# Kernel tuning notes

Measured on AMD Instinct MI355X. Metric: run time of the kernel, lower is better.

## Reference

```python
import jax, jax.numpy as jnp
import numpy as np

B, C_IN, T_IN = 128, 128, 2500
C_OUT, K, STRIDE, PAD = 64, 27, 4, 13  # T_out = 625
BN_EPS = 1e-5
SURROGATE_ALPHA = 4.0


def binarize_weight(w):
    """1-bit (XNOR-Net style) weight quantization with straight-through estimator.
    w: (O, I, K). Per-output-channel scale = mean |w|."""
    alpha = jnp.mean(jnp.abs(w), axis=(1, 2), keepdims=True)
    wq = jnp.sign(w) * alpha
    return w + jax.lax.stop_gradient(wq - w)


def spike(x):
    """Heaviside spike with sigmoid surrogate gradient (STE)."""
    hard = (x > 0).astype(x.dtype)
    soft = jax.nn.sigmoid(SURROGATE_ALPHA * x)
    return soft + jax.lax.stop_gradient(hard - soft)


def setup_inputs() -> dict:
    key = jax.random.key(0)
    ks = jax.random.split(key, 8)
    scale_conv = 1.0 / np.sqrt(C_IN * K)
    scale_lin = 1.0 / np.sqrt(C_OUT)
    return {
        "x": jax.random.normal(ks[0], (B, C_IN, T_IN), dtype=jnp.float32),
        "conv_w": jax.random.normal(ks[1], (C_OUT, C_IN, K), dtype=jnp.float32) * scale_conv,
        "conv_b": jnp.zeros((C_OUT,), dtype=jnp.float32),
        "bn_gamma": jnp.ones((C_OUT,), dtype=jnp.float32),
        "bn_beta": jnp.zeros((C_OUT,), dtype=jnp.float32),
        "bn_mean": jax.random.normal(ks[2], (C_OUT,), dtype=jnp.float32) * 0.1,
        "bn_var": jax.random.uniform(ks[3], (C_OUT,), dtype=jnp.float32, minval=0.5, maxval=1.5),
        "wq": jax.random.normal(ks[4], (C_OUT, C_OUT), dtype=jnp.float32) * scale_lin,
        "wk": jax.random.normal(ks[5], (C_OUT, C_OUT), dtype=jnp.float32) * scale_lin,
        "wv": jax.random.normal(ks[6], (C_OUT, C_OUT), dtype=jnp.float32) * scale_lin,
        "wo": jax.random.normal(ks[7], (C_OUT, C_OUT), dtype=jnp.float32) * scale_lin,
    }


def reference(x, conv_w, conv_b, bn_gamma, bn_beta, bn_mean, bn_var, wq, wk, wv, wo):
    # --- 1-bit quantized conv1d, stride 4 ---
    w_bin = binarize_weight(conv_w)
    y = jax.lax.conv_general_dilated(
        x, w_bin, window_strides=(STRIDE,), padding=[(PAD, PAD)],
        dimension_numbers=("NCH", "OIH", "NCH"))
    y = y + conv_b[None, :, None]  # (B, C_OUT, 625)

    # --- BatchNorm1d (inference stats) + ELU ---
    inv = jax.lax.rsqrt(bn_var + BN_EPS)
    y = (y - bn_mean[None, :, None]) * (inv * bn_gamma)[None, :, None] + bn_beta[None, :, None]
    y = jax.nn.elu(y)

    # --- Global spiking attention (single head) ---
    s = spike(y)                                   # (B, C, T) binary spikes
    q = jnp.einsum("oc,bct->bot", wq, s)           # (B, C, T)
    k = jnp.einsum("oc,bct->bot", wk, s)
    v = jnp.einsum("oc,bct->bot", wv, y)
    scores = jnp.einsum("bct,bcs->bts", q, k) / jnp.sqrt(jnp.asarray(C_OUT, y.dtype))
    attn = jax.nn.softmax(scores, axis=-1)         # (B, T, T)
    ctx = jnp.einsum("bts,bcs->bct", attn, v)      # (B, C, T)
    out = y + jnp.einsum("oc,bct->bot", wo, ctx)   # residual
    return out
```

## Files before the change

kernel.cpp:

```cpp
#include <hip/hip_runtime.h>
#include <math.h>

#define B_    128
#define CIN   128
#define TIN   2500
#define COUT  64
#define KW    27
#define TOUT  625
#define TPAD  640
#define CTT   32
#define GROWS 152

typedef __bf16 bf16x8 __attribute__((ext_vector_type(8)));
typedef float  f32x4  __attribute__((ext_vector_type(4)));

__device__ __forceinline__ unsigned short f32_to_bf16_rne(float v) {
    unsigned u = __float_as_uint(v);
    u += 0x7FFFu + ((u >> 16) & 1u);
    return (unsigned short)(u >> 16);
}

__device__ __forceinline__ f32x4 mfma_bf16(bf16x8 a, bf16x8 b, f32x4 c) {
    return __builtin_amdgcn_mfma_f32_16x16x32_bf16(a, b, c, 0, 0, 0);
}

__device__ __forceinline__ bf16x8 expand_sgn(unsigned b) {
    union { unsigned u[4]; bf16x8 v; } r;
#pragma unroll
    for (int j = 0; j < 4; j++) {
        unsigned lo = (b >> (2 * j)) & 1u;
        unsigned hi = (b >> (2 * j + 1)) & 1u;
        r.u[j] = 0x3F803F80u | (lo << 15) | (hi << 31);
    }
    return r.v;
}

__global__ void binarize_kernel(const float* __restrict__ w,
                                unsigned* __restrict__ sgn2,
                                float* __restrict__ alpha_out) {
    int o = blockIdx.x, tid = threadIdx.x;
    __shared__ float red[256];
    const float* wo_ = w + (size_t)o * (CIN * KW);
    float s = 0.f;
    for (int idx = tid; idx < CIN * KW; idx += 256) s += fabsf(wo_[idx]);
    red[tid] = s;
    __syncthreads();
    for (int st = 128; st > 0; st >>= 1) {
        if (tid < st) red[tid] += red[tid + st];
        __syncthreads();
    }
    if (tid == 0) alpha_out[o] = red[0] / (float)(CIN * KW);

    for (int t = tid; t < KW * 4; t += 256) {
        int kk = t >> 2, kg = t & 3;
        unsigned u = 0;
#pragma unroll
        for (int cs = 0; cs < 4; cs++) {
#pragma unroll
            for (int j = 0; j < 8; j++) {
                int c = cs * 32 + kg * 8 + j;
                float v = wo_[c * KW + kk];
                unsigned bit = (v > 0.f) ? 0u : 1u;
                u |= bit << (cs * 8 + j);
            }
        }
        sgn2[(kk * 4 + kg) * 64 + o] = u;
    }
}

__global__ void transpose_w_kernel(const float* __restrict__ wq, const float* __restrict__ wk,
                                   const float* __restrict__ wv, const float* __restrict__ wo,
                                   const float* __restrict__ conv_b, const float* __restrict__ gamma_,
                                   const float* __restrict__ beta_, const float* __restrict__ mean_,
                                   const float* __restrict__ var_, const float* __restrict__ alpha_,
                                   float* __restrict__ dstT,
                                   unsigned short* __restrict__ wo_h, unsigned short* __restrict__ wo_l,
                                   float* __restrict__ scA, float* __restrict__ scB) {
    if (blockIdx.x < 3) {
        const float* srcs[3] = {wq, wk, wv};
        const float* src = srcs[blockIdx.x];
        float* dst = dstT + (size_t)blockIdx.x * 4096;
        for (int idx = threadIdx.x; idx < 4096; idx += 256) {
            int o = idx >> 6, c = idx & 63;
            dst[c * 64 + o] = src[idx];
        }
    } else if (blockIdx.x == 3) {
        for (int idx = threadIdx.x; idx < 4096; idx += 256) {
            float v = wo[idx];
            unsigned short h = f32_to_bf16_rne(v);
            float hf = __uint_as_float((unsigned)h << 16);
            wo_h[idx] = h;
            wo_l[idx] = f32_to_bf16_rne(v - hf);
        }
    } else {
        int o = threadIdx.x;
        if (o < 64) {
            float inv = rsqrtf(var_[o] + 1e-5f);
            float G = gamma_[o] * inv;
            scA[o] = alpha_[o] * G;
            scB[o] = (conv_b[o] - mean_[o]) * G + beta_[o];
        }
    }
}

__global__ __launch_bounds__(256, 4) void conv_kernel(
    const float* __restrict__ x, const unsigned* __restrict__ sgn2,
    const float* __restrict__ scA, const float* __restrict__ scB,
    float* __restrict__ y_out)
{
    __shared__ __align__(16) unsigned short xhi[GROWS * 128];

    int b = blockIdx.y;
    int t0 = blockIdx.x * CTT;
    int tid = threadIdx.x;

    const float* xb = x + (size_t)b * CIN * TIN;
    int gbase = 4 * t0 - 13;
    for (int task = tid; task < 16 * GROWS; task += 256) {
        int c8 = task / GROWS, gl = task - c8 * GROWS;
        int g = gbase + gl;
        bool valid = (gl < 151) && ((unsigned)g < (unsigned)TIN);
        float vs[8];
#pragma unroll
        for (int j = 0; j < 8; j++)
            vs[j] = valid ? xb[(size_t)(c8 * 8 + j) * TIN + g] : 0.f;
        union { unsigned u[4]; uint4 q; } H;
#pragma unroll
        for (int j = 0; j < 4; j++) {
            unsigned short h0 = f32_to_bf16_rne(vs[2 * j]);
            unsigned short h1 = f32_to_bf16_rne(vs[2 * j + 1]);
            H.u[j] = (unsigned)h0 | ((unsigned)h1 << 16);
        }
        int c8p = c8 ^ ((gl >> 2) & 15);
        *(uint4*)(xhi + gl * 128 + c8p * 8) = H.q;
    }
    __syncthreads();

    int wave = tid >> 6, lane = tid & 63;
    int o0 = wave * 16;
    int n = lane & 15, kg = lane >> 4;

    f32x4 acc0 = {0.f, 0.f, 0.f, 0.f};
    f32x4 acc1 = {0.f, 0.f, 0.f, 0.f};

    const unsigned* sgb = sgn2 + (size_t)kg * 64 + o0 + n;
    unsigned sa = sgb[0];

#pragma unroll 1
    for (int kk = 0; kk < KW; ++kk) {
        unsigned na = 0;
        if (kk < KW - 1) na = sgb[(kk + 1) * 256];
        int gl = 4 * n + kk;
        int rot = (gl >> 2) & 15;
        const unsigned short* xr0 = xhi + gl * 128;
        const unsigned short* xr1 = xr0 + 8192;
#pragma unroll
        for (int cs = 0; cs < 4; ++cs) {
            int c8p = (cs * 4 + kg) ^ rot;
            bf16x8 b0 = *(const bf16x8*)(xr0 + c8p * 8);
            bf16x8 b1 = *(const bf16x8*)(xr1 + c8p * 8);
            bf16x8 a = expand_sgn((sa >> (8 * cs)) & 0xFFu);
            acc0 = mfma_bf16(a, b0, acc0);
            acc1 = mfma_bf16(a, b1, acc1);
        }
        sa = na;
    }

    int quad = lane >> 4, col = lane & 15;
#pragma unroll
    for (int tt = 0; tt < 2; ++tt) {
        int t_g = t0 + tt * 16 + col;
        if (t_g < TOUT) {
            f32x4 a = tt ? acc1 : acc0;
#pragma unroll
            for (int r = 0; r < 4; ++r) {
                int o = o0 + quad * 4 + r;
                float s = a[r] * scA[o] + scB[o];
                float yv = s > 0.f ? s : expm1f(s);
                y_out[((size_t)b * COUT + o) * TOUT + t_g] = yv;
            }
        }
    }
}

__global__ __launch_bounds__(256, 2) void proj_kernel(
    const float* __restrict__ y, const float* __restrict__ wqT,
    const float* __restrict__ wkT, const float* __restrict__ wvT,
    unsigned short* __restrict__ q_h, unsigned short* __restrict__ k_h,
    unsigned short* __restrict__ vT_h)
{
    __shared__ float w_sh[3 * 4096];
    __shared__ __align__(16) float y_sh[64 * 72];
    int b = blockIdx.y, t0 = blockIdx.x * 64, tid = threadIdx.x;

    for (int i = tid; i < 4096; i += 256) {
        w_sh[i]         = wqT[i];
        w_sh[4096 + i]  = wkT[i];
        w_sh[8192 + i]  = wvT[i];
    }
    const float* yb = y + (size_t)b * COUT * TOUT;
    for (int i = tid; i < 64 * 64; i += 256) {
        int c = i >> 6, tt = i & 63;
        int t = t0 + tt;
        y_sh[c * 72 + tt] = (t < TOUT) ? yb[c * TOUT + t] : 0.f;
    }
    __syncthreads();

    int oo = tid & 63, tq = tid >> 6;
    float q[16], k[16], v[16];
#pragma unroll
    for (int j = 0; j < 16; j++) { q[j] = 0.f; k[j] = 0.f; v[j] = 0.f; }

#pragma unroll 1
    for (int c = 0; c < 64; ++c) {
        float wq = w_sh[c * 64 + oo];
        float wk = w_sh[4096 + c * 64 + oo];
        float wv = w_sh[8192 + c * 64 + oo];
        const float* yr = &y_sh[c * 72 + tq * 16];
#pragma unroll
        for (int j4 = 0; j4 < 4; ++j4) {
            float4 y4 = *(const float4*)(yr + 4 * j4);
            float ys[4] = {y4.x, y4.y, y4.z, y4.w};
#pragma unroll
            for (int j = 0; j < 4; ++j) {
                float yv = ys[j];
                float sp = yv > 0.f ? 1.f : 0.f;
                q[4 * j4 + j] += wq * sp;
                k[4 * j4 + j] += wk * sp;
                v[4 * j4 + j] += wv * yv;
            }
        }
    }

    int tbase = t0 + tq * 16;
#pragma unroll
    for (int j = 0; j < 16; ++j) {
        size_t off = ((size_t)b * TPAD + tbase + j) * 64 + oo;
        q_h[off] = f32_to_bf16_rne(q[j]);
        k_h[off] = f32_to_bf16_rne(k[j]);
    }
    union { unsigned short u[16]; uint4 q4[2]; } V;
#pragma unroll
    for (int j = 0; j < 16; ++j) V.u[j] = f32_to_bf16_rne(v[j]);
    unsigned short* vp = vT_h + ((size_t)b * 64 + oo) * TPAD + tbase;
    ((uint4*)vp)[0] = V.q4[0];
    ((uint4*)vp)[1] = V.q4[1];
}

__global__ __launch_bounds__(512, 3) void attn_kernel(
    const unsigned short* __restrict__ q_h, const unsigned short* __restrict__ k_h,
    const unsigned short* __restrict__ vT_h, const float* __restrict__ y,
    const unsigned short* __restrict__ wo_h, const unsigned short* __restrict__ wo_l,
    float* __restrict__ out)
{
    __shared__ float sc_sh[16 * 648];
    __shared__ float ctx_sh[2 * 64 * 17];
    __shared__ float red_sh[512];
    __shared__ float rden[16];

    int b = blockIdx.y, t0 = blockIdx.x * 16, tid = threadIdx.x;
    int wave = tid >> 6, lane = tid & 63;
    int quad = lane >> 4, nlo = lane & 15;

    const unsigned short* qb = q_h + ((size_t)b * TPAD + t0 + nlo) * 64 + quad * 8;
    bf16x8 qa0 = *(const bf16x8*)(qb);
    bf16x8 qa1 = *(const bf16x8*)(qb + 32);
    const unsigned short* kbase = k_h + (size_t)b * TPAD * 64 + quad * 8;
#pragma unroll 5
    for (int nt = 0; nt < 5; ++nt) {
        int s = wave * 80 + nt * 16 + nlo;
        const unsigned short* krow = kbase + (size_t)s * 64;
        bf16x8 kb0 = *(const bf16x8*)(krow);
        bf16x8 kb1 = *(const bf16x8*)(krow + 32);
        f32x4 acc = {0.f, 0.f, 0.f, 0.f};
        acc = mfma_bf16(qa0, kb0, acc);
        acc = mfma_bf16(qa1, kb1, acc);
#pragma unroll
        for (int r = 0; r < 4; ++r)
            sc_sh[(quad * 4 + r) * 648 + s] = acc[r] * 0.125f;
    }
    __syncthreads();

    int ti1 = tid >> 5, sg = tid & 31;
    float mx = -3.0e38f;
    for (int s = sg; s < TOUT; s += 32) mx = fmaxf(mx, sc_sh[ti1 * 648 + s]);
    red_sh[tid] = mx;
    __syncthreads();
    float rowm = red_sh[ti1 * 32];
#pragma unroll
    for (int l = 1; l < 32; l++) rowm = fmaxf(rowm, red_sh[ti1 * 32 + l]);
    __syncthreads();
    float sum = 0.f;
    for (int s = sg; s < TOUT; s += 32) {
        float e = __expf(sc_sh[ti1 * 648 + s] - rowm);
        sc_sh[ti1 * 648 + s] = e;
        sum += e;
    }
    red_sh[tid] = sum;
    __syncthreads();
    if (tid < 16) {
        float tot = 0.f;
#pragma unroll
        for (int l = 0; l < 32; l++) tot += red_sh[tid * 32 + l];
        rden[tid] = 1.f / tot;
    }
    __syncthreads();

    int cw = (wave & 3) * 16, kh = wave >> 2;
    const unsigned short* vb = vT_h + ((size_t)b * 64 + cw + nlo) * TPAD;
    f32x4 cacc = {0.f, 0.f, 0.f, 0.f};
    int ks0 = kh * 10;
#pragma unroll 5
    for (int i = 0; i < 10; ++i) {
        int ks = ks0 + i;
        const float* pr = &sc_sh[nlo * 648 + ks * 32 + quad * 8];
        union { unsigned short u[8]; bf16x8 v; } P;
#pragma unroll
        for (int j = 0; j < 8; ++j) P.u[j] = f32_to_bf16_rne(pr[j]);
        bf16x8 v8 = *(const bf16x8*)(vb + ks * 32 + quad * 8);
        cacc = mfma_bf16(P.v, v8, cacc);
    }
#pragma unroll
    for (int r = 0; r < 4; ++r)
        ctx_sh[kh * 1088 + (cw + nlo) * 17 + quad * 4 + r] = cacc[r] * rden[quad * 4 + r];
    __syncthreads();

    if (wave < 4) {
        const unsigned short* woh = wo_h + (size_t)(wave * 16 + nlo) * 64 + quad * 8;
        const unsigned short* wol = wo_l + (size_t)(wave * 16 + nlo) * 64 + quad * 8;
        f32x4 oacc = {0.f, 0.f, 0.f, 0.f};
#pragma unroll
        for (int ks = 0; ks < 2; ++ks) {
            union { unsigned short u[8]; bf16x8 v; } Bc;
#pragma unroll
            for (int j = 0; j < 8; ++j) {
                int c = ks * 32 + quad * 8 + j;
                float cv = ctx_sh[c * 17 + nlo] + ctx_sh[1088 + c * 17 + nlo];
                Bc.u[j] = f32_to_bf16_rne(cv);
            }
            bf16x8 ah = *(const bf16x8*)(woh + ks * 32);
            bf16x8 al = *(const bf16x8*)(wol + ks * 32);
            oacc = mfma_bf16(ah, Bc.v, oacc);
            oacc = mfma_bf16(al, Bc.v, oacc);
        }
        int t_g = t0 + nlo;
        if (t_g < TOUT) {
#pragma unroll
            for (int r = 0; r < 4; ++r) {
                int o = wave * 16 + quad * 4 + r;
                size_t off = ((size_t)b * COUT + o) * TOUT + t_g;
                out[off] = y[off] + oacc[r];
            }
        }
    }
}

extern "C" void kernel_launch(void* const* d_in, const int* in_sizes, int n_in,
                              void* d_out, int out_size, void* d_ws, size_t ws_size,
                              hipStream_t stream) {
    const float* x        = (const float*)d_in[0];
    const float* conv_w   = (const float*)d_in[1];
    const float* conv_b   = (const float*)d_in[2];
    const float* bn_gamma = (const float*)d_in[3];
    const float* bn_beta  = (const float*)d_in[4];
    const float* bn_mean  = (const float*)d_in[5];
    const float* bn_var   = (const float*)d_in[6];
    const float* wq       = (const float*)d_in[7];
    const float* wk       = (const float*)d_in[8];
    const float* wv       = (const float*)d_in[9];
    const float* wo       = (const float*)d_in[10];
    float* out = (float*)d_out;
    float* ws  = (float*)d_ws;

    unsigned* sgn2        = (unsigned*)ws;
    float* alpha          = ws + 110592;
    float* scA            = ws + 110656;
    float* scB            = ws + 110720;
    float* wT4            = ws + 110848;
    unsigned short* wo_h  = (unsigned short*)(ws + 123136);
    unsigned short* wo_l  = (unsigned short*)(ws + 125184);
    float* yb             = ws + 131072;
    unsigned short* q_h   = (unsigned short*)(ws + 5251072);
    unsigned short* k_h   = (unsigned short*)(ws + 7872512);
    unsigned short* vT_h  = (unsigned short*)(ws + 10493952);

    hipLaunchKernelGGL(binarize_kernel, dim3(64), dim3(256), 0, stream, conv_w, sgn2, alpha);
    hipLaunchKernelGGL(transpose_w_kernel, dim3(5), dim3(256), 0, stream,
                       wq, wk, wv, wo, conv_b, bn_gamma, bn_beta, bn_mean, bn_var, alpha,
                       wT4, wo_h, wo_l, scA, scB);
    hipLaunchKernelGGL(conv_kernel, dim3(20, 128), dim3(256), 0, stream,
                       x, sgn2, scA, scB, yb);
    hipLaunchKernelGGL(proj_kernel, dim3(10, 128), dim3(256), 0, stream,
                       yb, wT4, wT4 + 4096, wT4 + 8192, q_h, k_h, vT_h);
    hipLaunchKernelGGL(attn_kernel, dim3(40, 128), dim3(512), 0, stream,
                       q_h, k_h, vT_h, yb, wo_h, wo_l, out);
}
```

Baseline: 494.3 us.

## Use sign LUT for conv weights and fuse softmax bf16 packing with shuffle reductions

In the conv kernel, the per-MFMA bit-expansion of weight signs is replaced with two 64-bit lookups into a 16-entry shared-memory table. In the attention kernel, the row max and sum reductions now use wave shuffles instead of shared-memory arrays and extra barriers. The exponentials are written back as packed bf16 in place, so the P·V loop loads ready bf16x8 vectors instead of converting floats. This trims ALU work and barriers, at the cost of extra LDS reads in the conv inner loop and in-place aliasing of the score buffer.

```diff
diff --git a/kernel.cpp b/kernel.cpp
--- a/kernel.cpp
+++ b/kernel.cpp
@@ -22,17 +22,6 @@
 
 __device__ __forceinline__ f32x4 mfma_bf16(bf16x8 a, bf16x8 b, f32x4 c) {
     return __builtin_amdgcn_mfma_f32_16x16x32_bf16(a, b, c, 0, 0, 0);
-}
-
-__device__ __forceinline__ bf16x8 expand_sgn(unsigned b) {
-    union { unsigned u[4]; bf16x8 v; } r;
-#pragma unroll
-    for (int j = 0; j < 4; j++) {
-        unsigned lo = (b >> (2 * j)) & 1u;
-        unsigned hi = (b >> (2 * j + 1)) & 1u;
-        r.u[j] = 0x3F803F80u | (lo << 15) | (hi << 31);
-    }
-    return r.v;
 }
 
 __global__ void binarize_kernel(const float* __restrict__ w,
@@ -109,10 +98,21 @@
     float* __restrict__ y_out)
 {
     __shared__ __align__(16) unsigned short xhi[GROWS * 128];
+    __shared__ __align__(16) unsigned long long sgnlut[16];
 
     int b = blockIdx.y;
     int t0 = blockIdx.x * CTT;
     int tid = threadIdx.x;
+
+    if (tid < 16) {
+        unsigned long long e = 0;
+#pragma unroll
+        for (int j = 0; j < 4; ++j) {
+            unsigned long long h = ((tid >> j) & 1) ? 0xBF80ull : 0x3F80ull;
+            e |= h << (16 * j);
+        }
+        sgnlut[tid] = e;
+    }
 
     const float* xb = x + (size_t)b * CIN * TIN;
     int gbase = 4 * t0 - 13;
@@ -159,9 +159,12 @@
             int c8p = (cs * 4 + kg) ^ rot;
             bf16x8 b0 = *(const bf16x8*)(xr0 + c8p * 8);
             bf16x8 b1 = *(const bf16x8*)(xr1 + c8p * 8);
-            bf16x8 a = expand_sgn((sa >> (8 * cs)) & 0xFFu);
-            acc0 = mfma_bf16(a, b0, acc0);
-            acc1 = mfma_bf16(a, b1, acc1);
+            unsigned byte = (sa >> (8 * cs)) & 0xFFu;
+            union { unsigned long long u[2]; bf16x8 v; } A;
+            A.u[0] = sgnlut[byte & 15u];
+            A.u[1] = sgnlut[byte >> 4];
+            acc0 = mfma_bf16(A.v, b0, acc0);
+            acc1 = mfma_bf16(A.v, b1, acc1);
         }
         sa = na;
     }
@@ -253,9 +256,8 @@
     const unsigned short* __restrict__ wo_h, const unsigned short* __restrict__ wo_l,
     float* __restrict__ out)
 {
-    __shared__ float sc_sh[16 * 648];
+    __shared__ __align__(16) float sc_sh[16 * 648];
     __shared__ float ctx_sh[2 * 64 * 17];
-    __shared__ float red_sh[512];
     __shared__ float rden[16];
 
     int b = blockIdx.y, t0 = blockIdx.x * 16, tid = threadIdx.x;
@@ -282,43 +284,41 @@
     __syncthreads();
 
     int ti1 = tid >> 5, sg = tid & 31;
+    float* srow = &sc_sh[ti1 * 648];
     float mx = -3.0e38f;
-    for (int s = sg; s < TOUT; s += 32) mx = fmaxf(mx, sc_sh[ti1 * 648 + s]);
-    red_sh[tid] = mx;
-    __syncthreads();
-    float rowm = red_sh[ti1 * 32];
-#pragma unroll
-    for (int l = 1; l < 32; l++) rowm = fmaxf(rowm, red_sh[ti1 * 32 + l]);
-    __syncthreads();
+    for (int s = sg; s < TOUT; s += 32) mx = fmaxf(mx, srow[s]);
+#pragma unroll
+    for (int off = 16; off >= 1; off >>= 1) mx = fmaxf(mx, __shfl_xor(mx, off));
+
+    unsigned short* prow = (unsigned short*)srow;
     float sum = 0.f;
-    for (int s = sg; s < TOUT; s += 32) {
-        float e = __expf(sc_sh[ti1 * 648 + s] - rowm);
-        sc_sh[ti1 * 648 + s] = e;
-        sum += e;
-    }
-    red_sh[tid] = sum;
-    __syncthreads();
-    if (tid < 16) {
-        float tot = 0.f;
-#pragma unroll
-        for (int l = 0; l < 32; l++) tot += red_sh[tid * 32 + l];
-        rden[tid] = 1.f / tot;
-    }
+#pragma unroll
+    for (int k2 = 0; k2 < 10; ++k2) {
+        int s = 2 * sg + 64 * k2;
+        float2 v2 = *(const float2*)(srow + s);
+        float e0 = (s     < TOUT) ? __expf(v2.x - mx) : 0.f;
+        float e1 = (s + 1 < TOUT) ? __expf(v2.y - mx) : 0.f;
+        sum += e0 + e1;
+        unsigned u0 = __float_as_uint(e0); u0 += 0x7FFFu + ((u0 >> 16) & 1u);
+        unsigned u1 = __float_as_uint(e1); u1 += 0x7FFFu + ((u1 >> 16) & 1u);
+        *(unsigned*)(prow + s) = (u0 >> 16) | (u1 & 0xFFFF0000u);
+    }
+#pragma unroll
+    for (int off = 16; off >= 1; off >>= 1) sum += __shfl_xor(sum, off);
+    if (sg == 0) rden[ti1] = 1.f / sum;
     __syncthreads();
 
     int cw = (wave & 3) * 16, kh = wave >> 2;
     const unsigned short* vb = vT_h + ((size_t)b * 64 + cw + nlo) * TPAD;
+    const unsigned short* pb = (const unsigned short*)sc_sh + nlo * 1296;
     f32x4 cacc = {0.f, 0.f, 0.f, 0.f};
     int ks0 = kh * 10;
 #pragma unroll 5
     for (int i = 0; i < 10; ++i) {
         int ks = ks0 + i;
-        const float* pr = &sc_sh[nlo * 648 + ks * 32 + quad * 8];
-        union { unsigned short u[8]; bf16x8 v; } P;
-#pragma unroll
-        for (int j = 0; j < 8; ++j) P.u[j] = f32_to_bf16_rne(pr[j]);
+        bf16x8 pv = *(const bf16x8*)(pb + ks * 32 + quad * 8);
         bf16x8 v8 = *(const bf16x8*)(vb + ks * 32 + quad * 8);
-        cacc = mfma_bf16(P.v, v8, cacc);
+        cacc = mfma_bf16(pv, v8, cacc);
     }
 #pragma unroll
     for (int r = 0; r < 4; ++r)
```

Result: faster. 478.2 us (-3.3%).
